# Performance work log

Hardware: AMD Instinct MI355X
Metric: run time of the kernel (lower is better)

## Reference

```python
import jax, jax.numpy as jnp
import numpy as np
from jax import lax

B, T, I, H, O = 1000, 100, 264, 100, 264


def _lstm_cell(x, h, c, Wih, Whh, bih, bhh):
    # PyTorch gate order: i, f, g, o
    gates = x @ Wih.T + bih + h @ Whh.T + bhh  # [B, 4H]
    i, f, g, o = jnp.split(gates, 4, axis=-1)
    i = jax.nn.sigmoid(i)
    f = jax.nn.sigmoid(f)
    g = jnp.tanh(g)
    o = jax.nn.sigmoid(o)
    c = f * c + i * g
    h = o * jnp.tanh(c)
    return h, c


def _encode(src, Wih, Whh, bih, bhh):
    # src: [B, T, I] -> final (h, c), each [B, H]
    x_t = jnp.swapaxes(src, 0, 1)  # [T, B, I]
    h0 = jnp.zeros((src.shape[0], H), src.dtype)
    c0 = jnp.zeros((src.shape[0], H), src.dtype)

    def step(carry, x):
        h, c = carry
        h, c = _lstm_cell(x, h, c, Wih, Whh, bih, bhh)
        return (h, c), None

    (h, c), _ = lax.scan(step, (h0, c0), x_t)
    return h, c


def _decode(h, c, Wih, Whh, bih, bhh, fcW, fcb, batch, steps):
    x0 = jnp.zeros((batch, I), h.dtype)

    def step(carry, _):
        x, hh, cc = carry
        hh, cc = _lstm_cell(x, hh, cc, Wih, Whh, bih, bhh)
        pred = hh @ fcW.T + fcb  # [B, O]
        return (pred, hh, cc), pred

    _, preds = lax.scan(step, (x0, h, c), None, length=steps)
    return jnp.swapaxes(preds, 0, 1)  # [B, T, O]


def setup_inputs():
    key = jax.random.key(0)
    ks = jax.random.split(key, 20)
    bound = 1.0 / np.sqrt(H)

    def u(k, shp):
        return jax.random.uniform(k, shp, jnp.float32, -bound, bound)

    inp = {
        "src": jax.random.normal(ks[0], (B, T, I), jnp.float32),
        "trg": jax.random.normal(ks[1], (B, T, I), jnp.float32),
        "enc_Wih": u(ks[2], (4 * H, I)), "enc_Whh": u(ks[3], (4 * H, H)),
        "enc_bih": u(ks[4], (4 * H,)), "enc_bhh": u(ks[5], (4 * H,)),
        "pd_Wih": u(ks[6], (4 * H, I)), "pd_Whh": u(ks[7], (4 * H, H)),
        "pd_bih": u(ks[8], (4 * H,)), "pd_bhh": u(ks[9], (4 * H,)),
        "pd_fcW": u(ks[10], (O, H)), "pd_fcb": u(ks[11], (O,)),
        "rd_Wih": u(ks[12], (4 * H, I)), "rd_Whh": u(ks[13], (4 * H, H)),
        "rd_bih": u(ks[14], (4 * H,)), "rd_bhh": u(ks[15], (4 * H,)),
        "rd_fcW": u(ks[16], (O, H)), "rd_fcb": u(ks[17], (O,)),
    }
    return inp


def reference(src, trg, enc_Wih, enc_Whh, enc_bih, enc_bhh,
              pd_Wih, pd_Whh, pd_bih, pd_bhh, pd_fcW, pd_fcb,
              rd_Wih, rd_Whh, rd_bih, rd_bhh, rd_fcW, rd_fcb):
    batch, steps, _ = src.shape
    h, c = _encode(src, enc_Wih, enc_Whh, enc_bih, enc_bhh)

    predict_output = _decode(h, c, pd_Wih, pd_Whh, pd_bih, pd_bhh,
                             pd_fcW, pd_fcb, batch, steps)
    predict_loss = jnp.mean((predict_output - trg) ** 2)

    reconstruct_output = _decode(h, c, rd_Wih, rd_Whh, rd_bih, rd_bhh,
                                 rd_fcW, rd_fcb, batch, steps)
    src_rev = src[:, ::-1, :]
    reconstruct_loss = jnp.mean((reconstruct_output - src_rev) ** 2)

    return reconstruct_loss, predict_loss
```

## Files before the change

### kernel.cpp

```cpp
#include <hip/hip_runtime.h>
#include <math.h>

#define NB 1000
#define NT 100
#define NI 264
#define NH 100
#define NO 264
#define NG 400
#define KE 364
#define DM 4
#define NDB 250
#define EDM 4
#define DTH 704
#define XM 16

__device__ __forceinline__ float sigm(float x){ return 1.f / (1.f + __expf(-x)); }
__device__ __forceinline__ float tanh_fast(float x){
    float e = __expf(-2.f * x);
    return 2.f / (1.f + e) - 1.f;
}

#define FMA4(acc, hv, wv) acc += hv.x*wv.x + hv.y*wv.y + hv.z*wv.z + hv.w*wv.w;

#define W_LIST(OP) OP(0) OP(1) OP(2) OP(3) OP(4) OP(5) OP(6) OP(7) OP(8) OP(9) \
                   OP(10) OP(11) OP(12) OP(13) OP(14) OP(15) OP(16) OP(17) OP(18) OP(19) \
                   OP(20) OP(21) OP(22) OP(23) OP(24)

#define DECL_W(i)    float4 w##i = make_float4(0.f, 0.f, 0.f, 0.f);
#define LOADW_ENC(i) w##i = WhhT4[(i) * NG + n];

#define ROW4K(wv, kk) { float4 hq; \
    hq = ((const float4*)sh_h[0])[kk]; FMA4(a0, hq, wv) \
    hq = ((const float4*)sh_h[1])[kk]; FMA4(a1, hq, wv) \
    hq = ((const float4*)sh_h[2])[kk]; FMA4(a2, hq, wv) \
    hq = ((const float4*)sh_h[3])[kk]; FMA4(a3, hq, wv) }

#define ESTEP(i) ROW4K(w##i, i)

#define ROW4(wq) { float4 hq; \
    hq = ((const float4*)sh_h[0])[k4]; FMA4(a0, hq, wq) \
    hq = ((const float4*)sh_h[1])[k4]; FMA4(a1, hq, wq) \
    hq = ((const float4*)sh_h[2])[k4]; FMA4(a2, hq, wq) \
    hq = ((const float4*)sh_h[3])[k4]; FMA4(a3, hq, wq) }


__global__ void prep_T4(const float* __restrict__ in, float* __restrict__ out, int N, int K)
{
    int idx = blockIdx.x * 256 + threadIdx.x;
    if (idx >= N * K) return;
    int j  = idx & 3;
    int n  = (idx >> 2) % N;
    int k  = (idx / (4 * N)) * 4 + j;
    out[idx] = in[n * K + k];
}

__global__ void prep_encT(const float* __restrict__ Wih, const float* __restrict__ Whh,
                          float* __restrict__ out)
{
    int idx = blockIdx.x * 256 + threadIdx.x;
    if (idx >= NG * KE) return;
    int j  = idx & 3;
    int n  = (idx >> 2) % NG;
    int k  = (idx / (4 * NG)) * 4 + j;
    out[idx] = (k < NI) ? Wih[n * NI + k] : Whh[n * NH + (k - NI)];
}

__global__ void prep_wdec(const float* __restrict__ Wih, const float* __restrict__ Whh,
                          const float* __restrict__ fcW, float* __restrict__ WdecT)
{
    int idx = blockIdx.x * 256 + threadIdx.x;
    if (idx >= NG * NH) return;
    int n = idx / NH, k = idx - n * NH;
    float acc = Whh[idx];
    const float* wr = Wih + (size_t)n * NI;
    for (int o = 0; o < NI; ++o) acc = fmaf(wr[o], fcW[o * NH + k], acc);
    WdecT[((k >> 2) * NG + n) * 4 + (k & 3)] = acc;
}

__global__ void prep_bias(const float* __restrict__ pb1, const float* __restrict__ pb2,
                          const float* __restrict__ pW,  const float* __restrict__ pfb,
                          const float* __restrict__ rb1, const float* __restrict__ rb2,
                          const float* __restrict__ rW,  const float* __restrict__ rfb,
                          const float* __restrict__ eb1, const float* __restrict__ eb2,
                          float* __restrict__ b0_p, float* __restrict__ bdec_p,
                          float* __restrict__ b0_r, float* __restrict__ bdec_r,
                          float* __restrict__ bcat, float* __restrict__ loss)
{
    int tid = blockIdx.x * 256 + threadIdx.x;
    if (tid < 2) loss[tid] = 0.f;
    if (tid < NG) bcat[tid] = eb1[tid] + eb2[tid];
    if (tid >= 2 * NG) return;
    int dd = tid / NG, n = tid - dd * NG;
    const float* b1 = dd ? rb1 : pb1;
    const float* b2 = dd ? rb2 : pb2;
    const float* W  = dd ? rW  : pW;
    const float* fb = dd ? rfb : pfb;
    float base = b1[n] + b2[n];
    float acc = base;
    const float* wr = W + (size_t)n * NI;
    for (int o = 0; o < NI; ++o) acc = fmaf(wr[o], fb[o], acc);
    if (dd){ b0_r[n] = base; bdec_r[n] = acc; }
    else   { b0_p[n] = base; bdec_p[n] = acc; }
}


__global__ __launch_bounds__(512) void xp_kernel(const float* __restrict__ src,
                                                 const float4* __restrict__ WihT4,
                                                 float* __restrict__ xp)
{
    __shared__ float sh_x[XM * NI];
    __shared__ float sh_o[XM * NG];
    const int tid = threadIdx.x;
    const size_t bt0 = (size_t)blockIdx.x * XM;
    for (int i = tid; i < XM * NI; i += 512) sh_x[i] = src[bt0 * NI + i];
    __syncthreads();
    const bool act = tid < NG;
    const int n = act ? tid : 0;
    float a0=0,a1=0,a2=0,a3=0,a4=0,a5=0,a6=0,a7=0,
          a8=0,a9=0,a10=0,a11=0,a12=0,a13=0,a14=0,a15=0;
    if (act){
        #pragma unroll 3
        for (int k4 = 0; k4 < NI / 4; ++k4){
            float4 wq = WihT4[k4 * NG + n];
            float4 hq;
            #define XROW(r, acc) hq = ((const float4*)(sh_x + (r) * NI))[k4]; FMA4(acc, hq, wq)
            XROW(0,a0)  XROW(1,a1)  XROW(2,a2)  XROW(3,a3)
            XROW(4,a4)  XROW(5,a5)  XROW(6,a6)  XROW(7,a7)
            XROW(8,a8)  XROW(9,a9)  XROW(10,a10) XROW(11,a11)
            XROW(12,a12) XROW(13,a13) XROW(14,a14) XROW(15,a15)
            #undef XROW
        }
        sh_o[0*NG+n]=a0;   sh_o[1*NG+n]=a1;   sh_o[2*NG+n]=a2;   sh_o[3*NG+n]=a3;
        sh_o[4*NG+n]=a4;   sh_o[5*NG+n]=a5;   sh_o[6*NG+n]=a6;   sh_o[7*NG+n]=a7;
        sh_o[8*NG+n]=a8;   sh_o[9*NG+n]=a9;   sh_o[10*NG+n]=a10; sh_o[11*NG+n]=a11;
        sh_o[12*NG+n]=a12; sh_o[13*NG+n]=a13; sh_o[14*NG+n]=a14; sh_o[15*NG+n]=a15;
    }
    __syncthreads();
    for (int i = tid; i < XM * NG; i += 512) xp[bt0 * NG + i] = sh_o[i];
}


__global__ __launch_bounds__(512) __attribute__((amdgpu_waves_per_eu(2, 2)))
void enc_rec(const float* __restrict__ xp,
             const float4* __restrict__ WhhT4,
             const float* __restrict__ bcat,
             float* __restrict__ h_out, float* __restrict__ c_out)
{
    __shared__ float sh_h[EDM][104];
    __shared__ float sh_g[NG][EDM + 1];
    const int tid = threadIdx.x;
    const int b0  = blockIdx.x * EDM;
    const bool act = tid < NG;
    const int n  = act ? tid : 0;
    const int mc = n / NH, jc = n % NH;
    float bias = act ? bcat[n] : 0.f;
    float c0 = 0.f;

    W_LIST(DECL_W)
    if (act){
        W_LIST(LOADW_ENC)
        sh_h[mc][jc] = 0.f;
    }
    __syncthreads();

    for (int t = 0; t < NT; ++t){
        if (act){
            const float* xr = xp + ((size_t)b0 * NT + t) * NG + n;
            float a0 = bias + xr[0 * NT * NG];
            float a1 = bias + xr[1 * NT * NG];
            float a2 = bias + xr[2 * NT * NG];
            float a3 = bias + xr[3 * NT * NG];
            W_LIST(ESTEP)
            sh_g[n][0]=a0; sh_g[n][1]=a1; sh_g[n][2]=a2; sh_g[n][3]=a3;
        }
        __syncthreads();
        if (act){
            float ai = sh_g[jc][mc], af = sh_g[NH + jc][mc];
            float ag = sh_g[2*NH + jc][mc], ao = sh_g[3*NH + jc][mc];
            float ii = sigm(ai), ff = sigm(af), gg = tanh_fast(ag), oo = sigm(ao);
            c0 = ff * c0 + ii * gg;
            sh_h[mc][jc] = oo * tanh_fast(c0);
        }
        __syncthreads();
    }
    if (act){
        h_out[(size_t)(b0 + mc) * NH + jc] = sh_h[mc][jc];
        c_out[(size_t)(b0 + mc) * NH + jc] = c0;
    }
}


__global__ __launch_bounds__(512) void enc_stream(const float* __restrict__ src,
                                                  const float4* __restrict__ WencT4,
                                                  const float* __restrict__ bcat,
                                                  float* __restrict__ h_out, float* __restrict__ c_out)
{
    __shared__ float sh_xh[4][368];
    __shared__ float sh_g[NG][5];
    const int tid = threadIdx.x;
    const int m0  = blockIdx.x * 4;
    const bool act = tid < NG;
    const int n  = act ? tid : 0;
    const int mc = n / NH, jc = n % NH;
    float bias = act ? bcat[n] : 0.f;
    float c_reg = 0.f, h_new = 0.f;
    if (act) sh_xh[mc][NI + jc] = 0.f;
    const float* s0 = src + (size_t)m0 * NT * NI;

    for (int t = 0; t < NT; ++t){
        for (int i = tid; i < 4 * NI; i += 512){
            int r = i / NI, k = i - r * NI;
            sh_xh[r][k] = s0[(size_t)r * NT * NI + (size_t)t * NI + k];
        }
        __syncthreads();
        if (act){
            float a0 = bias, a1 = bias, a2 = bias, a3 = bias;
            #pragma unroll 7
            for (int k4 = 0; k4 < KE / 4; ++k4){
                float4 wq = WencT4[k4 * NG + n];
                float4 hq;
                hq = ((const float4*)sh_xh[0])[k4]; FMA4(a0, hq, wq)
                hq = ((const float4*)sh_xh[1])[k4]; FMA4(a1, hq, wq)
                hq = ((const float4*)sh_xh[2])[k4]; FMA4(a2, hq, wq)
                hq = ((const float4*)sh_xh[3])[k4]; FMA4(a3, hq, wq)
            }
            sh_g[n][0]=a0; sh_g[n][1]=a1; sh_g[n][2]=a2; sh_g[n][3]=a3;
        }
        __syncthreads();
        if (act){
            float ai = sh_g[jc][mc], af = sh_g[NH + jc][mc];
            float ag = sh_g[2*NH + jc][mc], ao = sh_g[3*NH + jc][mc];
            float ii = sigm(ai), ff = sigm(af), gg = tanh_fast(ag), oo = sigm(ao);
            c_reg = ff * c_reg + ii * gg;
            h_new = oo * tanh_fast(c_reg);
            sh_xh[mc][NI + jc] = h_new;
        }
        __syncthreads();
    }
    if (act){
        h_out[(size_t)(m0 + mc) * NH + jc] = h_new;
        c_out[(size_t)(m0 + mc) * NH + jc] = c_reg;
    }
}


__global__ __launch_bounds__(DTH) void decoder_kernel(
    const float* __restrict__ h_enc, const float* __restrict__ c_enc,
    const float4* __restrict__ WhhT_p, const float4* __restrict__ WdecT_p,
    const float* __restrict__ b0_p,  const float* __restrict__ bdec_p,
    const float4* __restrict__ fcWT_p, const float* __restrict__ fcb_p,
    const float* __restrict__ trg,
    const float4* __restrict__ WhhT_r, const float4* __restrict__ WdecT_r,
    const float* __restrict__ b0_r,  const float* __restrict__ bdec_r,
    const float4* __restrict__ fcWT_r, const float* __restrict__ fcb_r,
    const float* __restrict__ src,
    float* __restrict__ loss)
{
    __shared__ float sh_h[DM][104];
    __shared__ float sh_g[NG][DM + 1];
    __shared__ float sh_red[11];
    const int tid = threadIdx.x;
    const int d   = (blockIdx.x >= NDB) ? 1 : 0;
    const int m0  = (blockIdx.x - d * NDB) * DM;
    const float4* WhhT  = d ? WhhT_r  : WhhT_p;
    const float4* WdecT = d ? WdecT_r : WdecT_p;
    const float*  b0    = d ? b0_r    : b0_p;
    const float*  bdec  = d ? bdec_r  : bdec_p;
    const float4* fcWT  = d ? fcWT_r  : fcWT_p;
    const float*  fcb   = d ? fcb_r   : fcb_p;
    const float*  tgt   = d ? src     : trg;

    const bool gate = tid < NG;
    const bool fc   = (tid >= NG) && (tid < NG + NO);
    const int n  = gate ? tid : 0;
    const int o  = fc ? tid - NG : 0;
    const int mc = n / NH, jc = n % NH;

    float b0n = 0.f, bdn = 0.f, fb = 0.f;
    if (gate){ b0n = b0[n]; bdn = bdec[n]; }
    else if (fc){ fb = fcb[o]; }

    float c0 = 0.f;
    if (gate){
        c0 = c_enc[(size_t)(m0 + mc) * NH + jc];
        sh_h[mc][jc] = h_enc[(size_t)(m0 + mc) * NH + jc];
    }
    float loss_acc = 0.f;
    __syncthreads();

    for (int k = 0; k <= NT; ++k){
        float a0, a1, a2, a3;
        if (gate && k < NT){
            const float4* WT = (k == 0) ? WhhT : WdecT;
            float bb = k ? bdn : b0n;
            a0=bb; a1=bb; a2=bb; a3=bb;
            #pragma unroll 5
            for (int k4 = 0; k4 < NH / 4; ++k4){
                float4 wq = WT[k4 * NG + n];
                ROW4(wq)
            }
            sh_g[n][0]=a0; sh_g[n][1]=a1; sh_g[n][2]=a2; sh_g[n][3]=a3;
        } else if (fc && k >= 1){
            a0=fb; a1=fb; a2=fb; a3=fb;
            #pragma unroll 5
            for (int k4 = 0; k4 < NH / 4; ++k4){
                float4 wq = fcWT[k4 * NO + o];
                ROW4(wq)
            }
            const int ti = d ? (NT - k) : (k - 1);
            const float* tg = tgt + (size_t)m0 * NT * NI + (size_t)ti * NI + o;
            float df;
            df = a0 - tg[0 * NT * NI]; loss_acc += df * df;
            df = a1 - tg[1 * NT * NI]; loss_acc += df * df;
            df = a2 - tg[2 * NT * NI]; loss_acc += df * df;
            df = a3 - tg[3 * NT * NI]; loss_acc += df * df;
        }
        __syncthreads();
        if (gate && k < NT){
            float ai = sh_g[jc][mc], af = sh_g[NH + jc][mc];
            float ag = sh_g[2*NH + jc][mc], ao = sh_g[3*NH + jc][mc];
            float ii = sigm(ai), ff = sigm(af), gg = tanh_fast(ag), oo = sigm(ao);
            c0 = ff * c0 + ii * gg;
            sh_h[mc][jc] = oo * tanh_fast(c0);
        }
        __syncthreads();
    }

    for (int off = 32; off > 0; off >>= 1) loss_acc += __shfl_down(loss_acc, off);
    if ((tid & 63) == 0) sh_red[tid >> 6] = loss_acc;
    __syncthreads();
    if (tid == 0){
        float s = 0.f;
        for (int w = 0; w < 11; ++w) s += sh_red[w];
        atomicAdd(&loss[d], s);
    }
}

__global__ void finalize_kernel(const float* __restrict__ loss, float* __restrict__ out){
    if (threadIdx.x == 0){
        const float inv = 1.f / 26400000.f;
        out[0] = loss[1] * inv;
        out[1] = loss[0] * inv;
    }
}

extern "C" void kernel_launch(void* const* d_in, const int* in_sizes, int n_in,
                              void* d_out, int out_size, void* d_ws, size_t ws_size,
                              hipStream_t stream)
{
    const float* src  = (const float*)d_in[0];
    const float* trg  = (const float*)d_in[1];
    const float* eWih = (const float*)d_in[2];
    const float* eWhh = (const float*)d_in[3];
    const float* ebih = (const float*)d_in[4];
    const float* ebhh = (const float*)d_in[5];
    const float* pWih = (const float*)d_in[6];
    const float* pWhh = (const float*)d_in[7];
    const float* pbih = (const float*)d_in[8];
    const float* pbhh = (const float*)d_in[9];
    const float* pfcW = (const float*)d_in[10];
    const float* pfcb = (const float*)d_in[11];
    const float* rWih = (const float*)d_in[12];
    const float* rWhh = (const float*)d_in[13];
    const float* rbih = (const float*)d_in[14];
    const float* rbhh = (const float*)d_in[15];
    const float* rfcW = (const float*)d_in[16];
    const float* rfcb = (const float*)d_in[17];

    float* w       = (float*)d_ws;
    float* WihT4e  = w;
    float* WencT4  = w + 105600;
    float* WhhT4e  = w + 251200;
    float* WdT_p   = w + 291200;
    float* WdT_r   = w + 331200;
    float* WhT_p   = w + 371200;
    float* WhT_r   = w + 411200;
    float* fcT_p   = w + 451200;
    float* fcT_r   = w + 477600;
    float* b0_p    = w + 504000;
    float* bdec_p  = w + 504400;
    float* b0_r    = w + 504800;
    float* bdec_r  = w + 505200;
    float* bcat    = w + 505600;
    float* h_enc   = w + 506000;
    float* c_enc   = w + 606000;
    float* loss    = w + 706000;
    float* XP      = w + 706016;
    const bool big = ws_size >= (size_t)(706016 + 40000000) * 4;

    const int TB = 256;
    if (big){
        prep_T4<<<(NG*NI + TB-1)/TB, TB, 0, stream>>>(eWih, WihT4e, NG, NI);
        prep_T4<<<(NG*NH + TB-1)/TB, TB, 0, stream>>>(eWhh, WhhT4e, NG, NH);
    } else {
        prep_encT<<<(NG*KE + TB-1)/TB, TB, 0, stream>>>(eWih, eWhh, WencT4);
    }
    prep_T4<<<(NG*NH + TB-1)/TB, TB, 0, stream>>>(pWhh, WhT_p, NG, NH);
    prep_T4<<<(NG*NH + TB-1)/TB, TB, 0, stream>>>(rWhh, WhT_r, NG, NH);
    prep_T4<<<(NO*NH + TB-1)/TB, TB, 0, stream>>>(pfcW, fcT_p, NO, NH);
    prep_T4<<<(NO*NH + TB-1)/TB, TB, 0, stream>>>(rfcW, fcT_r, NO, NH);
    prep_wdec<<<(NG*NH + TB-1)/TB, TB, 0, stream>>>(pWih, pWhh, pfcW, WdT_p);
    prep_wdec<<<(NG*NH + TB-1)/TB, TB, 0, stream>>>(rWih, rWhh, rfcW, WdT_r);
    prep_bias<<<4, TB, 0, stream>>>(pbih, pbhh, pWih, pfcb, rbih, rbhh, rWih, rfcb,
                                    ebih, ebhh, b0_p, bdec_p, b0_r, bdec_r, bcat, loss);

    if (big){
        xp_kernel<<<(NB*NT)/XM, 512, 0, stream>>>(src, (const float4*)WihT4e, XP);
        enc_rec<<<NB/EDM, 512, 0, stream>>>(XP, (const float4*)WhhT4e, bcat, h_enc, c_enc);
    } else {
        enc_stream<<<NB/4, 512, 0, stream>>>(src, (const float4*)WencT4, bcat, h_enc, c_enc);
    }
    decoder_kernel<<<2 * NDB, DTH, 0, stream>>>(h_enc, c_enc,
        (const float4*)WhT_p, (const float4*)WdT_p, b0_p, bdec_p, (const float4*)fcT_p, pfcb, trg,
        (const float4*)WhT_r, (const float4*)WdT_r, b0_r, bdec_r, (const float4*)fcT_r, rfcb, src,
        loss);
    finalize_kernel<<<1, 64, 0, stream>>>(loss, (float*)d_out);
}
```

Measured before the change: 2.227 ms.

## Shrink decoder blocks to 192 threads with four gates per thread

The decoder kernel drops from 704 threads to 192. Each gate thread now computes all four gate rows (i, f, g, o) for one hidden unit across the four batch rows and keeps four cell states in registers. A single 64-thread wave handles the FC projection, with five output columns per thread. This reuses each shared-memory h load across more FMAs and makes the barriers cheaper. In exchange, each thread does more serial work per step and uses more registers.

```diff
diff --git a/kernel.cpp b/kernel.cpp
--- a/kernel.cpp
+++ b/kernel.cpp
@@ -11,7 +11,7 @@
 #define DM 4
 #define NDB 250
 #define EDM 4
-#define DTH 704
+#define DTH 192
 #define XM 16
 
 __device__ __forceinline__ float sigm(float x){ return 1.f / (1.f + __expf(-x)); }
@@ -36,12 +36,6 @@
     hq = ((const float4*)sh_h[3])[kk]; FMA4(a3, hq, wv) }
 
 #define ESTEP(i) ROW4K(w##i, i)
-
-#define ROW4(wq) { float4 hq; \
-    hq = ((const float4*)sh_h[0])[k4]; FMA4(a0, hq, wq) \
-    hq = ((const float4*)sh_h[1])[k4]; FMA4(a1, hq, wq) \
-    hq = ((const float4*)sh_h[2])[k4]; FMA4(a2, hq, wq) \
-    hq = ((const float4*)sh_h[3])[k4]; FMA4(a3, hq, wq) }
 
 
 __global__ void prep_T4(const float* __restrict__ in, float* __restrict__ out, int N, int K)
@@ -258,7 +252,7 @@
 {
     __shared__ float sh_h[DM][104];
     __shared__ float sh_g[NG][DM + 1];
-    __shared__ float sh_red[11];
+    __shared__ float sh_red[3];
     const int tid = threadIdx.x;
     const int d   = (blockIdx.x >= NDB) ? 1 : 0;
     const int m0  = (blockIdx.x - d * NDB) * DM;
@@ -270,58 +264,125 @@
     const float*  fcb   = d ? fcb_r   : fcb_p;
     const float*  tgt   = d ? src     : trg;
 
-    const bool gate = tid < NG;
-    const bool fc   = (tid >= NG) && (tid < NG + NO);
+    const bool gate = tid < NH;
+    const bool fc   = (tid >= 128) && (tid < 192);
     const int n  = gate ? tid : 0;
-    const int o  = fc ? tid - NG : 0;
-    const int mc = n / NH, jc = n % NH;
-
-    float b0n = 0.f, bdn = 0.f, fb = 0.f;
-    if (gate){ b0n = b0[n]; bdn = bdec[n]; }
-    else if (fc){ fb = fcb[o]; }
-
-    float c0 = 0.f;
+    const int o  = fc ? tid - 128 : 0;
+    const bool fcx = fc && (o < 8);
+
+    float bz0=0,bz1=0,bz2=0,bz3=0, bd0=0,bd1=0,bd2=0,bd3=0;
+    float fb0=0,fb1=0,fb2=0,fb3=0,fb4=0;
     if (gate){
-        c0 = c_enc[(size_t)(m0 + mc) * NH + jc];
-        sh_h[mc][jc] = h_enc[(size_t)(m0 + mc) * NH + jc];
+        bz0=b0[n];        bz1=b0[n+NH];     bz2=b0[n+2*NH];   bz3=b0[n+3*NH];
+        bd0=bdec[n];      bd1=bdec[n+NH];   bd2=bdec[n+2*NH]; bd3=bdec[n+3*NH];
+    } else if (fc){
+        fb0=fcb[o]; fb1=fcb[o+64]; fb2=fcb[o+128]; fb3=fcb[o+192];
+        if (fcx) fb4=fcb[o+256];
+    }
+
+    float c0=0.f, c1=0.f, c2=0.f, c3=0.f;
+    if (gate){
+        c0 = c_enc[(size_t)(m0+0)*NH + n];
+        c1 = c_enc[(size_t)(m0+1)*NH + n];
+        c2 = c_enc[(size_t)(m0+2)*NH + n];
+        c3 = c_enc[(size_t)(m0+3)*NH + n];
+        sh_h[0][n] = h_enc[(size_t)(m0+0)*NH + n];
+        sh_h[1][n] = h_enc[(size_t)(m0+1)*NH + n];
+        sh_h[2][n] = h_enc[(size_t)(m0+2)*NH + n];
+        sh_h[3][n] = h_enc[(size_t)(m0+3)*NH + n];
     }
     float loss_acc = 0.f;
     __syncthreads();
 
     for (int k = 0; k <= NT; ++k){
-        float a0, a1, a2, a3;
         if (gate && k < NT){
             const float4* WT = (k == 0) ? WhhT : WdecT;
-            float bb = k ? bdn : b0n;
-            a0=bb; a1=bb; a2=bb; a3=bb;
+            float biasA = k ? bd0 : bz0, biasB = k ? bd1 : bz1;
+            float biasC = k ? bd2 : bz2, biasD = k ? bd3 : bz3;
+            float A0=biasA,A1=biasA,A2=biasA,A3=biasA;
+            float B0=biasB,B1=biasB,B2=biasB,B3=biasB;
+            float C0=biasC,C1=biasC,C2=biasC,C3=biasC;
+            float D0=biasD,D1=biasD,D2=biasD,D3=biasD;
             #pragma unroll 5
             for (int k4 = 0; k4 < NH / 4; ++k4){
-                float4 wq = WT[k4 * NG + n];
-                ROW4(wq)
+                float4 wa = WT[k4 * NG + n];
+                float4 wb = WT[k4 * NG + n + NH];
+                float4 wc = WT[k4 * NG + n + 2*NH];
+                float4 wd = WT[k4 * NG + n + 3*NH];
+                float4 h0q = ((const float4*)sh_h[0])[k4];
+                float4 h1q = ((const float4*)sh_h[1])[k4];
+                float4 h2q = ((const float4*)sh_h[2])[k4];
+                float4 h3q = ((const float4*)sh_h[3])[k4];
+                FMA4(A0,h0q,wa) FMA4(A1,h1q,wa) FMA4(A2,h2q,wa) FMA4(A3,h3q,wa)
+                FMA4(B0,h0q,wb) FMA4(B1,h1q,wb) FMA4(B2,h2q,wb) FMA4(B3,h3q,wb)
+                FMA4(C0,h0q,wc) FMA4(C1,h1q,wc) FMA4(C2,h2q,wc) FMA4(C3,h3q,wc)
+                FMA4(D0,h0q,wd) FMA4(D1,h1q,wd) FMA4(D2,h2q,wd) FMA4(D3,h3q,wd)
             }
-            sh_g[n][0]=a0; sh_g[n][1]=a1; sh_g[n][2]=a2; sh_g[n][3]=a3;
+            sh_g[n][0]=A0;        sh_g[n][1]=A1;        sh_g[n][2]=A2;        sh_g[n][3]=A3;
+            sh_g[n+NH][0]=B0;     sh_g[n+NH][1]=B1;     sh_g[n+NH][2]=B2;     sh_g[n+NH][3]=B3;
+            sh_g[n+2*NH][0]=C0;   sh_g[n+2*NH][1]=C1;   sh_g[n+2*NH][2]=C2;   sh_g[n+2*NH][3]=C3;
+            sh_g[n+3*NH][0]=D0;   sh_g[n+3*NH][1]=D1;   sh_g[n+3*NH][2]=D2;   sh_g[n+3*NH][3]=D3;
         } else if (fc && k >= 1){
-            a0=fb; a1=fb; a2=fb; a3=fb;
+            float P0=fb0,P1=fb0,P2=fb0,P3=fb0;
+            float Q0=fb1,Q1=fb1,Q2=fb1,Q3=fb1;
+            float R0=fb2,R1=fb2,R2=fb2,R3=fb2;
+            float S0=fb3,S1=fb3,S2=fb3,S3=fb3;
+            float T0=fb4,T1=fb4,T2=fb4,T3=fb4;
             #pragma unroll 5
             for (int k4 = 0; k4 < NH / 4; ++k4){
-                float4 wq = fcWT[k4 * NO + o];
-                ROW4(wq)
+                float4 wa = fcWT[k4 * NO + o];
+                float4 wb = fcWT[k4 * NO + o + 64];
+                float4 wc = fcWT[k4 * NO + o + 128];
+                float4 wd = fcWT[k4 * NO + o + 192];
+                float4 h0q = ((const float4*)sh_h[0])[k4];
+                float4 h1q = ((const float4*)sh_h[1])[k4];
+                float4 h2q = ((const float4*)sh_h[2])[k4];
+                float4 h3q = ((const float4*)sh_h[3])[k4];
+                FMA4(P0,h0q,wa) FMA4(P1,h1q,wa) FMA4(P2,h2q,wa) FMA4(P3,h3q,wa)
+                FMA4(Q0,h0q,wb) FMA4(Q1,h1q,wb) FMA4(Q2,h2q,wb) FMA4(Q3,h3q,wb)
+                FMA4(R0,h0q,wc) FMA4(R1,h1q,wc) FMA4(R2,h2q,wc) FMA4(R3,h3q,wc)
+                FMA4(S0,h0q,wd) FMA4(S1,h1q,wd) FMA4(S2,h2q,wd) FMA4(S3,h3q,wd)
+                if (fcx){
+                    float4 we = fcWT[k4 * NO + o + 256];
+                    FMA4(T0,h0q,we) FMA4(T1,h1q,we) FMA4(T2,h2q,we) FMA4(T3,h3q,we)
+                }
             }
             const int ti = d ? (NT - k) : (k - 1);
-            const float* tg = tgt + (size_t)m0 * NT * NI + (size_t)ti * NI + o;
+            const float* tg = tgt + (size_t)m0 * NT * NI + (size_t)ti * NI;
             float df;
-            df = a0 - tg[0 * NT * NI]; loss_acc += df * df;
-            df = a1 - tg[1 * NT * NI]; loss_acc += df * df;
-            df = a2 - tg[2 * NT * NI]; loss_acc += df * df;
-            df = a3 - tg[3 * NT * NI]; loss_acc += df * df;
+            df = P0 - tg[0*NT*NI + o];       loss_acc += df * df;
+            df = P1 - tg[1*NT*NI + o];       loss_acc += df * df;
+            df = P2 - tg[2*NT*NI + o];       loss_acc += df * df;
+            df = P3 - tg[3*NT*NI + o];       loss_acc += df * df;
+            df = Q0 - tg[0*NT*NI + o + 64];  loss_acc += df * df;
+            df = Q1 - tg[1*NT*NI + o + 64];  loss_acc += df * df;
+            df = Q2 - tg[2*NT*NI + o + 64];  loss_acc += df * df;
+            df = Q3 - tg[3*NT*NI + o + 64];  loss_acc += df * df;
+            df = R0 - tg[0*NT*NI + o + 128]; loss_acc += df * df;
+            df = R1 - tg[1*NT*NI + o + 128]; loss_acc += df * df;
+            df = R2 - tg[2*NT*NI + o + 128]; loss_acc += df * df;
+            df = R3 - tg[3*NT*NI + o + 128]; loss_acc += df * df;
+            df = S0 - tg[0*NT*NI + o + 192]; loss_acc += df * df;
+            df = S1 - tg[1*NT*NI + o + 192]; loss_acc += df * df;
+            df = S2 - tg[2*NT*NI + o + 192]; loss_acc += df * df;
+            df = S3 - tg[3*NT*NI + o + 192]; loss_acc += df * df;
+            if (fcx){
+                df = T0 - tg[0*NT*NI + o + 256]; loss_acc += df * df;
+                df = T1 - tg[1*NT*NI + o + 256]; loss_acc += df * df;
+                df = T2 - tg[2*NT*NI + o + 256]; loss_acc += df * df;
+                df = T3 - tg[3*NT*NI + o + 256]; loss_acc += df * df;
+            }
         }
         __syncthreads();
         if (gate && k < NT){
-            float ai = sh_g[jc][mc], af = sh_g[NH + jc][mc];
-            float ag = sh_g[2*NH + jc][mc], ao = sh_g[3*NH + jc][mc];
-            float ii = sigm(ai), ff = sigm(af), gg = tanh_fast(ag), oo = sigm(ao);
-            c0 = ff * c0 + ii * gg;
-            sh_h[mc][jc] = oo * tanh_fast(c0);
+            #define ACT(r, cc) { \
+                float ai = sh_g[n][r], af = sh_g[NH + n][r]; \
+                float ag = sh_g[2*NH + n][r], ao = sh_g[3*NH + n][r]; \
+                float ii = sigm(ai), ff = sigm(af), gg = tanh_fast(ag), oo = sigm(ao); \
+                cc = ff * cc + ii * gg; \
+                sh_h[r][n] = oo * tanh_fast(cc); }
+            ACT(0, c0) ACT(1, c1) ACT(2, c2) ACT(3, c3)
+            #undef ACT
         }
         __syncthreads();
     }
@@ -330,8 +391,7 @@
     if ((tid & 63) == 0) sh_red[tid >> 6] = loss_acc;
     __syncthreads();
     if (tid == 0){
-        float s = 0.f;
-        for (int w = 0; w < 11; ++w) s += sh_red[w];
+        float s = sh_red[0] + sh_red[1] + sh_red[2];
         atomicAdd(&loss[d], s);
     }
 }
```

Result: slower. 2.290 ms (+2.8%).
